# Kernel tuning notes

Measured on AMD Instinct MI355X. Metric: run time of the kernel, lower is better.

Reference implementation:

```python
import jax, jax.numpy as jnp
import numpy as np
import math

B = 8; SEQ = 1000; C_IN = 32; D = 512; H = 8; DK = 64; DV = 64
DFF = 2048; NL = 4; ARY = 4; INNER = 5


def get_mask_np(seq_size, ary, inner):
    # full k-ary tree sizes (padded) and effective sizes per scale
    full = 1
    while full < seq_size:
        full *= ary
    all_size = [full]; effe = [seq_size]
    while all_size[-1] > 1:
        all_size.append(all_size[-1] // ary)
        effe.append(math.ceil(effe[-1] / ary))
    n = sum(all_size)
    allow = np.zeros((n, n), dtype=bool)
    w = inner // 2
    starts = np.concatenate([[0], np.cumsum(all_size)]).astype(int)
    # intra-scale local window
    for l, sz in enumerate(all_size):
        s = starts[l]
        for i in range(sz):
            lo = max(i - w, 0); hi = min(i + w + 1, sz)
            allow[s + i, s + lo:s + hi] = True
    # inter-scale parent<->children links
    for l in range(1, len(all_size)):
        s = starts[l]; ps = starts[l - 1]
        for i in range(all_size[l]):
            lo = ps + i * ary; hi = ps + (i + 1) * ary
            allow[s + i, lo:hi] = True
            allow[lo:hi, s + i] = True
    return allow, all_size, effe

ALLOW_NP, ALL_SIZE, EFFE_SIZE = get_mask_np(SEQ, ARY, INNER)
NTOT = sum(ALL_SIZE)   # 1365
DEPTH = len(ALL_SIZE)  # 6
OFFS = np.concatenate([[0], np.cumsum(ALL_SIZE)]).astype(int)


def sinusoid_pe(length, d):
    pos = np.arange(length)[:, None].astype(np.float64)
    i = np.arange(d)[None, :]
    ang = pos / np.power(10000.0, (2 * (i // 2)) / d)
    pe = np.zeros((length, d), np.float32)
    pe[:, 0::2] = np.sin(ang[:, 0::2]); pe[:, 1::2] = np.cos(ang[:, 1::2])
    return pe

PE_NP = sinusoid_pe(SEQ, D)


def layer_norm(x, s, b, eps=1e-5):
    m = x.mean(-1, keepdims=True)
    v = ((x - m) ** 2).mean(-1, keepdims=True)
    return (x - m) * jax.lax.rsqrt(v + eps) * s + b


def setup_inputs() -> dict:
    key = jax.random.key(0)
    ks = jax.random.split(key, 10)
    p = lambda k, shape, sc=0.02: jax.random.normal(k, shape, jnp.float32) * sc
    return {
        "x": jax.random.normal(ks[0], (B, SEQ, C_IN), jnp.float32),
        "conv_w": p(ks[1], (D, C_IN, 3), 0.05),
        "norm_s": jnp.ones((D,), jnp.float32), "norm_b": jnp.zeros((D,), jnp.float32),
        "wq": p(ks[2], (NL, D, H * DK)), "wk": p(ks[3], (NL, D, H * DK)),
        "wv": p(ks[4], (NL, D, H * DV)), "wo": p(ks[5], (NL, H * DV, D)),
        "ln1_s": jnp.ones((NL, D), jnp.float32), "ln1_b": jnp.zeros((NL, D), jnp.float32),
        "w1": p(ks[6], (NL, D, DFF)), "b1": jnp.zeros((NL, DFF), jnp.float32),
        "w2": p(ks[7], (NL, DFF, D)), "b2": jnp.zeros((NL, D), jnp.float32),
        "ln2_s": jnp.ones((NL, D), jnp.float32), "ln2_b": jnp.zeros((NL, D), jnp.float32),
    }


def reference(x, conv_w, norm_s, norm_b, wq, wk, wv, wo, ln1_s, ln1_b,
              w1, b1, w2, b2, ln2_s, ln2_b):
    allow = jnp.asarray(ALLOW_NP)        # [N,N] True = attend
    pe = jnp.asarray(PE_NP)              # [S,D]
    # --- DataEmbedding: conv1d(k=3, circular pad, no bias) + sinusoid PE ---
    xt = jnp.concatenate([x[:, -1:], x, x[:, :1]], axis=1)       # (B,S+2,C)
    emb = jax.lax.conv_general_dilated(
        xt, conv_w, (1,), 'VALID', dimension_numbers=('NWC', 'OIW', 'NWC'))
    emb = emb + pe[None]                                          # (B,S,D)
    # pad sequence to full-tree leaf count
    emb = jnp.pad(emb, ((0, 0), (0, ALL_SIZE[0] - SEQ), (0, 0)))  # (B,L0,D)
    # --- MaxPooling_Construct: pool by ary per level, concat, LayerNorm ---
    parts = [emb]
    cur = emb
    for lvl in range(DEPTH - 1):
        L = cur.shape[1]
        cur = cur.reshape(B, L // ARY, ARY, D).max(axis=2)
        parts.append(cur)
    seq = jnp.concatenate(parts, axis=1)                          # (B,N,D)
    seq = layer_norm(seq, norm_s, norm_b)
    # --- masked MHA encoder layers (post-norm) ---
    scale = 1.0 / math.sqrt(DK)
    neg = jnp.float32(-1e9)
    for l in range(NL):
        q = (seq @ wq[l]).reshape(B, NTOT, H, DK)
        k = (seq @ wk[l]).reshape(B, NTOT, H, DK)
        v = (seq @ wv[l]).reshape(B, NTOT, H, DV)
        scores = jnp.einsum('bnhd,bmhd->bhnm', q, k) * scale
        scores = jnp.where(allow[None, None], scores, neg)
        attn = jax.nn.softmax(scores, axis=-1)
        ctx = jnp.einsum('bhnm,bmhd->bnhd', attn, v).reshape(B, NTOT, H * DV)
        seq = layer_norm(seq + ctx @ wo[l], ln1_s[l], ln1_b[l])
        ff = jax.nn.gelu(seq @ w1[l] + b1[l], approximate=False) @ w2[l] + b2[l]
        seq = layer_norm(seq + ff, ln2_s[l], ln2_b[l])
    # --- keep only the effective (unpadded) prefix of each scale ---
    out = jnp.concatenate(
        [seq[:, OFFS[i]:OFFS[i] + EFFE_SIZE[i]] for i in range(DEPTH)], axis=1)
    return out  # (B, sum(effe)=1334, D)
```

## Files before the change

### kernel.cpp

```cpp
#include <hip/hip_runtime.h>
#include <cstdint>
#include <math.h>

#define DEV __device__ __forceinline__

static constexpr int BQ = 8, SEQN = 1000, CIN = 32, NH = 8;
static constexpr int NLAY = 4;
static constexpr int NTOT_C = 1365;
static constexpr int M_REAL = BQ * NTOT_C;
static constexpr int M_PAD  = 11008;

DEV float bf2f(unsigned short u){ return __uint_as_float(((unsigned)u) << 16); }
DEV unsigned short f2bf(float f){
  unsigned u = __float_as_uint(f);
  u += 0x7fffu + ((u >> 16) & 1u);
  return (unsigned short)(u >> 16);
}

typedef __bf16 bf16x8 __attribute__((ext_vector_type(8)));
typedef float  f32x4  __attribute__((ext_vector_type(4)));
typedef unsigned short u16x8 __attribute__((ext_vector_type(8)));

#define GLD_LDS16(gp, lp) __builtin_amdgcn_global_load_lds( \
    (const __attribute__((address_space(1))) void*)(gp), \
    (__attribute__((address_space(3))) void*)(lp), 16, 0, 0)

template<int N> DEV void waitcnt_vm(){
  asm volatile("s_waitcnt vmcnt(%0)" :: "i"(N) : "memory");
}
DEV void cfence(){ asm volatile("" ::: "memory"); }

__global__ __launch_bounds__(256) void pe_kernel(float* __restrict__ pe)
{
  int idx = blockIdx.x * 256 + threadIdx.x;
  int d = idx & 511, s = idx >> 9;
  if (s >= SEQN) return;
  float e2 = (float)(d & ~1);
  float freq = exp2f(e2 * (-13.287712379549449f / 512.0f));
  float ang = (float)s * freq;
  pe[idx] = (d & 1) ? cosf(ang) : sinf(ang);
}

__global__ __launch_bounds__(256) void conv_kernel(const float* __restrict__ x,
    const float* __restrict__ w, const float* __restrict__ pe, float* __restrict__ seqf)
{
  __shared__ float ws_w[128 * 97];
  __shared__ __align__(16) float xs[66][32];
  int b = blockIdx.z, s0 = blockIdx.y * 64, d0 = blockIdx.x * 128;
  int tid = threadIdx.x;
  for (int i = tid; i < 128 * 96; i += 256){
    int r = i / 96, c = i - r * 96;
    ws_w[r * 97 + c] = w[(size_t)(d0 + r) * 96 + c];
  }
  for (int i = tid; i < 66 * 32; i += 256){
    int r = i >> 5, c = i & 31;
    int ss = s0 + r - 1;
    ss = (ss < 0) ? (ss + SEQN) : (ss >= SEQN ? ss - SEQN : ss);
    xs[r][c] = x[((size_t)b * SEQN + ss) * CIN + c];
  }
  __syncthreads();
  int dl = tid & 127, sh = tid >> 7;
  float wr[96];
  #pragma unroll
  for (int i = 0; i < 96; i++) wr[i] = ws_w[dl * 97 + i];
  int d = d0 + dl;
  for (int si = 0; si < 32; si++){
    int sl = sh * 32 + si;
    int s = s0 + sl;
    float acc = 0.f;
    #pragma unroll
    for (int kk = 0; kk < 3; kk++){
      const float* xr = xs[sl + kk];
      #pragma unroll
      for (int c = 0; c < 32; c++) acc += xr[c] * wr[c * 3 + kk];
    }
    float outv = (s < SEQN) ? acc + pe[(size_t)s * 512 + d] : 0.f;
    seqf[((size_t)b * NTOT_C + s) * 512 + d] = outv;
  }
}

__global__ __launch_bounds__(256) void pool_kernel(float* __restrict__ seqf,
    int inOff, int outOff, int outSz)
{
  int e = blockIdx.x * 256 + threadIdx.x;
  int d = e & 511;
  int r = e >> 9;
  int i = r % outSz;
  int b = r / outSz;
  const float* src = seqf + ((size_t)b * NTOT_C + inOff + 4 * i) * 512 + d;
  float m = fmaxf(fmaxf(src[0], src[512]), fmaxf(src[1024], src[1536]));
  seqf[((size_t)b * NTOT_C + outOff + i) * 512 + d] = m;
}

template<bool RES>
__global__ __launch_bounds__(256) void ln_kernel(const float* __restrict__ xin,
    const float* __restrict__ rin, float* __restrict__ outf, unsigned short* __restrict__ outb,
    const float* __restrict__ sg, const float* __restrict__ bg, int M)
{
  int row = blockIdx.x;
  int t = threadIdx.x;
  size_t base = (size_t)row * 512;
  if (row >= M){ outb[base + t] = 0; outb[base + t + 256] = 0; return; }
  float v0 = xin[base + t], v1 = xin[base + t + 256];
  if (RES){ v0 += rin[base + t]; v1 += rin[base + t + 256]; }
  __shared__ float red1[4], red2[4];
  int wv = t >> 6;
  float sall = v0 + v1;
  #pragma unroll
  for (int o = 32; o; o >>= 1) sall += __shfl_xor(sall, o, 64);
  if ((t & 63) == 0) red1[wv] = sall;
  __syncthreads();
  float mean = (red1[0] + red1[1] + red1[2] + red1[3]) * (1.f / 512.f);
  float d0 = v0 - mean, d1 = v1 - mean;
  float sq = d0 * d0 + d1 * d1;
  #pragma unroll
  for (int o = 32; o; o >>= 1) sq += __shfl_xor(sq, o, 64);
  if ((t & 63) == 0) red2[wv] = sq;
  __syncthreads();
  float var = (red2[0] + red2[1] + red2[2] + red2[3]) * (1.f / 512.f);
  float rstd = 1.f / sqrtf(var + 1e-5f);
  float y0 = d0 * rstd * sg[t] + bg[t];
  float y1 = d1 * rstd * sg[t + 256] + bg[t + 256];
  outf[base + t] = y0; outf[base + t + 256] = y1;
  outb[base + t] = f2bf(y0); outb[base + t + 256] = f2bf(y1);
}

__global__ __launch_bounds__(256) void wconv_kernel(const float* __restrict__ w,
    unsigned short* __restrict__ wt, int K, int N, size_t sStride, size_t dStride)
{
  __shared__ float tile[32][33];
  const float* wl = w + blockIdx.z * sStride;
  unsigned short* wtl = wt + blockIdx.z * dStride;
  int n0 = blockIdx.x * 32, k0 = blockIdx.y * 32;
  int c = threadIdx.x & 31, r8 = threadIdx.x >> 5;
  #pragma unroll
  for (int p = 0; p < 4; p++){ int r = r8 + p * 8; tile[r][c] = wl[(size_t)(k0 + r) * N + n0 + c]; }
  __syncthreads();
  #pragma unroll
  for (int p = 0; p < 4; p++){ int r = r8 + p * 8; wtl[(size_t)(n0 + r) * K + k0 + c] = f2bf(tile[c][r]); }
}

template<int EPI, int MR, int NR>
__global__ __launch_bounds__(256) void gemm_kernel(
    const unsigned short* __restrict__ A, const unsigned short* __restrict__ Wt,
    float* __restrict__ Cf, unsigned short* __restrict__ Cb,
    const float* __restrict__ bias, const float* __restrict__ Rf, int N, int K)
{
  constexpr int BM = 32 * MR, BN = 32 * NR;
  constexpr int SLOT_A = BM * 32, SLOT_B = BN * 32;
  constexpr int L = MR / 2 + NR / 2;
  __shared__ __align__(16) unsigned short As[3][SLOT_A];
  __shared__ __align__(16) unsigned short Bs[3][SLOT_B];
  const int tid = threadIdx.x;
  const int wv = tid >> 6, lane = tid & 63;
  const int m0 = blockIdx.x * BM, n0 = blockIdx.y * BN;
  const int wm = (wv >> 1) * 16 * MR, wn = (wv & 1) * 16 * NR;
  const int r16 = lane & 15, g = lane >> 4;

  const int lrow = lane >> 2;
  const int scg  = (lane & 3) ^ ((lrow >> 1) & 3);
  const unsigned short* gA = A + (size_t)(m0 + 8 * MR * wv + lrow) * K + scg * 8;
  const unsigned short* gB = Wt + (size_t)(n0 + 8 * NR * wv + lrow) * K + scg * 8;
  const int lAoff = wv * 8 * MR * 32;
  const int lBoff = wv * 8 * NR * 32;

  f32x4 acc[MR][NR] = {};
  const int nt = K >> 5;

  auto STAGE = [&](int slot, int k0){
    #pragma unroll
    for (int ii = 0; ii < MR / 2; ii++)
      GLD_LDS16(gA + k0 + ii * 16 * K, &As[slot][lAoff + ii * 512]);
    #pragma unroll
    for (int ii = 0; ii < NR / 2; ii++)
      GLD_LDS16(gB + k0 + ii * 16 * K, &Bs[slot][lBoff + ii * 512]);
  };

  STAGE(0, 0);
  STAGE(1, 32);
  int cur = 0;
  const int rswz = (g ^ ((r16 >> 1) & 3)) * 8;
  for (int t = 0; t < nt; t++){
    int s2 = (cur == 0) ? 2 : cur - 1;
    if (t + 2 < nt) STAGE(s2, (t + 2) * 32);
    if (t + 2 < nt)      waitcnt_vm<2 * L>();
    else if (t + 1 < nt) waitcnt_vm<L>();
    else                 waitcnt_vm<0>();
    __builtin_amdgcn_s_barrier();
    cfence();
    bf16x8 av[MR], bv[NR];
    #pragma unroll
    for (int m = 0; m < MR; m++)
      av[m] = *reinterpret_cast<const bf16x8*>(&As[cur][(wm + m * 16 + r16) * 32 + rswz]);
    #pragma unroll
    for (int n = 0; n < NR; n++)
      bv[n] = *reinterpret_cast<const bf16x8*>(&Bs[cur][(wn + n * 16 + r16) * 32 + rswz]);
    __builtin_amdgcn_s_setprio(1);
    #pragma unroll
    for (int m = 0; m < MR; m++)
      #pragma unroll
      for (int n = 0; n < NR; n++)
        acc[m][n] = __builtin_amdgcn_mfma_f32_16x16x32_bf16(av[m], bv[n], acc[m][n], 0, 0, 0);
    __builtin_amdgcn_s_setprio(0);
    __builtin_amdgcn_s_barrier();
    cfence();
    cur = (cur == 2) ? 0 : cur + 1;
  }

  const int colBase = n0 + wn + r16;
  #pragma unroll
  for (int m = 0; m < MR; m++){
    int rowBase = m0 + wm + m * 16 + g * 4;
    #pragma unroll
    for (int n = 0; n < NR; n++){
      int col = colBase + n * 16;
      float bsv = (EPI >= 2) ? bias[col] : 0.f;
      #pragma unroll
      for (int j = 0; j < 4; j++){
        float vlu = acc[m][n][j];
        if (EPI >= 2) vlu += bsv;
        if (EPI == 2) vlu = 0.5f * vlu * (1.f + erff(vlu * 0.70710678118654752f));
        size_t off = (size_t)(rowBase + j) * N + col;
        if (EPI == 0 || EPI == 3) vlu += Rf[off];
        if (EPI == 1 || EPI == 2) Cb[off] = f2bf(vlu);
        else                      Cf[off] = vlu;
      }
    }
  }
}

__global__ __launch_bounds__(256) void attn_kernel(
    const unsigned short* __restrict__ qkv, unsigned short* __restrict__ ctx)
{
  int wid = blockIdx.x * 4 + (threadIdx.x >> 6);
  int lane = threadIdx.x & 63;
  int n = wid % NTOT_C;
  int b = wid / NTOT_C;

  int i, sz, of, cb, par;
  if (n < 1024){ i = n;        sz = 1024; of = 0;    cb = -1;            par = 1024 + (i >> 2); }
  else if (n < 1280){ i = n - 1024; sz = 256; of = 1024; cb = 0    + 4 * i; par = 1280 + (i >> 2); }
  else if (n < 1344){ i = n - 1280; sz = 64;  of = 1280; cb = 1024 + 4 * i; par = 1344 + (i >> 2); }
  else if (n < 1360){ i = n - 1344; sz = 16;  of = 1344; cb = 1280 + 4 * i; par = 1360 + (i >> 2); }
  else if (n < 1364){ i = n - 1360; sz = 4;   of = 1360; cb = 1344 + 4 * i; par = 1364; }
  else { i = 0; sz = 1; of = 1364; cb = 1360; par = -1; }

  int nb[10];
  #pragma unroll
  for (int s5 = 0; s5 < 5; s5++){ int pos = i - 2 + s5; nb[s5] = (pos >= 0 && pos < sz) ? of + pos : -1; }
  #pragma unroll
  for (int r = 0; r < 4; r++) nb[5 + r] = (cb >= 0) ? cb + r : -1;
  nb[9] = par;

  const unsigned short* rows = qkv + ((size_t)b * NTOT_C) * 1536;

  u16x8 qv = *reinterpret_cast<const u16x8*>(rows + (size_t)n * 1536 + lane * 8);
  float qf[8];
  #pragma unroll
  for (int e = 0; e < 8; e++) qf[e] = bf2f(qv[e]);

  float sc[10];
  #pragma unroll
  for (int j = 0; j < 10; j++){
    int id = nb[j] >= 0 ? nb[j] : n;
    u16x8 kv = *reinterpret_cast<const u16x8*>(rows + (size_t)id * 1536 + 512 + lane * 8);
    float p = 0.f;
    #pragma unroll
    for (int e = 0; e < 8; e++) p += qf[e] * bf2f(kv[e]);
    p += __shfl_xor(p, 1, 64);
    p += __shfl_xor(p, 2, 64);
    p += __shfl_xor(p, 4, 64);
    sc[j] = (nb[j] >= 0) ? p * 0.125f : -1e30f;
  }
  float mx = sc[0];
  #pragma unroll
  for (int j = 1; j < 10; j++) mx = fmaxf(mx, sc[j]);
  float den = 0.f;
  float wj[10];
  #pragma unroll
  for (int j = 0; j < 10; j++){
    wj[j] = (nb[j] >= 0) ? expf(sc[j] - mx) : 0.f;
    den += wj[j];
  }
  float rden = 1.f / den;
  float accv[8] = {};
  #pragma unroll
  for (int j = 0; j < 10; j++){
    int id = nb[j] >= 0 ? nb[j] : n;
    u16x8 vv = *reinterpret_cast<const u16x8*>(rows + (size_t)id * 1536 + 1024 + lane * 8);
    float w = wj[j];
    #pragma unroll
    for (int e = 0; e < 8; e++) accv[e] += w * bf2f(vv[e]);
  }
  u16x8 ov;
  #pragma unroll
  for (int e = 0; e < 8; e++) ov[e] = f2bf(accv[e] * rden);
  *reinterpret_cast<u16x8*>(ctx + ((size_t)b * NTOT_C + n) * 512 + lane * 8) = ov;
}

__global__ __launch_bounds__(256) void gather_kernel(const float* __restrict__ seqf,
    float* __restrict__ out)
{
  int e = blockIdx.x * 256 + threadIdx.x;
  int d = e & 511;
  int r = e >> 9;
  int j = r % 1334;
  int b = r / 1334;
  int src;
  if      (j < 1000) src = j;
  else if (j < 1250) src = j + 24;
  else if (j < 1313) src = j + 30;
  else if (j < 1333) src = j + 31;
  else               src = 1364;
  out[e] = seqf[((size_t)b * NTOT_C + src) * 512 + d];
}

extern "C" void kernel_launch(void* const* d_in, const int* in_sizes, int n_in,
                              void* d_out, int out_size, void* d_ws, size_t ws_size,
                              hipStream_t stream)
{
  const float* x      = (const float*)d_in[0];
  const float* conv_w = (const float*)d_in[1];
  const float* norm_s = (const float*)d_in[2];
  const float* norm_b = (const float*)d_in[3];
  const float* wq     = (const float*)d_in[4];
  const float* wk     = (const float*)d_in[5];
  const float* wv     = (const float*)d_in[6];
  const float* wo     = (const float*)d_in[7];
  const float* ln1_s  = (const float*)d_in[8];
  const float* ln1_b  = (const float*)d_in[9];
  const float* w1     = (const float*)d_in[10];
  const float* b1     = (const float*)d_in[11];
  const float* w2     = (const float*)d_in[12];
  const float* b2     = (const float*)d_in[13];
  const float* ln2_s  = (const float*)d_in[14];
  const float* ln2_b  = (const float*)d_in[15];
  float* out = (float*)d_out;

  char* ws = (char*)d_ws;
  size_t off = 0;
  auto alloc = [&](size_t bytes) -> char* {
    char* p = ws + off; off += (bytes + 255) & ~(size_t)255; return p;
  };
  unsigned short* qkvT = (unsigned short*)alloc((size_t)NLAY * 1536 * 512 * 2);
  unsigned short* woT  = (unsigned short*)alloc((size_t)NLAY * 512 * 512 * 2);
  unsigned short* w1T  = (unsigned short*)alloc((size_t)NLAY * 2048 * 512 * 2);
  unsigned short* w2T  = (unsigned short*)alloc((size_t)NLAY * 512 * 2048 * 2);
  float*          seqf = (float*)alloc((size_t)M_PAD * 512 * 4);
  unsigned short* seqb = (unsigned short*)alloc((size_t)M_PAD * 512 * 2);
  float*          buff = (float*)alloc((size_t)M_PAD * 512 * 4);
  unsigned short* qkvb = (unsigned short*)alloc((size_t)M_PAD * 1536 * 2);
  unsigned short* ctxb = (unsigned short*)alloc((size_t)M_PAD * 512 * 2);
  unsigned short* ffn1 = qkvb;
  float*          pe   = buff;

  wconv_kernel<<<dim3(16,16,NLAY),256,0,stream>>>(wq, qkvT,              512,  512,  (size_t)512*512,  (size_t)1536*512);
  wconv_kernel<<<dim3(16,16,NLAY),256,0,stream>>>(wk, qkvT + 512*512,    512,  512,  (size_t)512*512,  (size_t)1536*512);
  wconv_kernel<<<dim3(16,16,NLAY),256,0,stream>>>(wv, qkvT + 1024*512,   512,  512,  (size_t)512*512,  (size_t)1536*512);
  wconv_kernel<<<dim3(16,16,NLAY),256,0,stream>>>(wo, woT,               512,  512,  (size_t)512*512,  (size_t)512*512);
  wconv_kernel<<<dim3(64,16,NLAY),256,0,stream>>>(w1, w1T,               512,  2048, (size_t)512*2048, (size_t)512*2048);
  wconv_kernel<<<dim3(16,64,NLAY),256,0,stream>>>(w2, w2T,               2048, 512,  (size_t)2048*512, (size_t)2048*512);

  pe_kernel<<<(SEQN * 512) / 256, 256, 0, stream>>>(pe);
  conv_kernel<<<dim3(4,16,BQ), 256, 0, stream>>>(x, conv_w, pe, seqf);
  const int psz[6]  = {1024, 256, 64, 16, 4, 1};
  const int poff[6] = {0, 1024, 1280, 1344, 1360, 1364};
  for (int l = 0; l < 5; l++)
    pool_kernel<<<(BQ * psz[l+1] * 512) / 256, 256, 0, stream>>>(seqf, poff[l], poff[l+1], psz[l+1]);
  ln_kernel<false><<<M_PAD, 256, 0, stream>>>(seqf, nullptr, seqf, seqb, norm_s, norm_b, M_REAL);

  for (int l = 0; l < NLAY; l++){
    gemm_kernel<1,4,4><<<dim3(86,12),256,0,stream>>>(seqb, qkvT + (size_t)l*1536*512, nullptr, qkvb, nullptr, nullptr, 1536, 512);
    attn_kernel<<<(BQ * NTOT_C + 3) / 4, 256, 0, stream>>>(qkvb, ctxb);
    gemm_kernel<0,2,2><<<dim3(172,8),256,0,stream>>>(ctxb, woT + (size_t)l*512*512, buff, nullptr, nullptr, seqf, 512, 512);
    ln_kernel<false><<<M_PAD,256,0,stream>>>(buff, nullptr, seqf, seqb, ln1_s + l*512, ln1_b + l*512, M_REAL);
    gemm_kernel<2,4,4><<<dim3(86,16),256,0,stream>>>(seqb, w1T + (size_t)l*2048*512, nullptr, ffn1, b1 + l*2048, nullptr, 2048, 512);
    gemm_kernel<3,2,4><<<dim3(172,4),256,0,stream>>>(ffn1, w2T + (size_t)l*512*2048, buff, nullptr, b2 + l*512, seqf, 512, 2048);
    ln_kernel<false><<<M_PAD,256,0,stream>>>(buff, nullptr, seqf, seqb, ln2_s + l*512, ln2_b + l*512, M_REAL);
  }

  gather_kernel<<<(BQ * 1334 * 512) / 256, 256, 0, stream>>>(seqf, out);
}
```

Baseline: 838.9 us.

## Replace GEMMs with 256-row, 512-thread double-buffered kernel and tanh GELU

Replaces the templated 3-stage GEMM with a larger-tile kernel: 256-row by up to 256-column tiles, 8 waves, K-step 64 with double buffering and split A/B prefetch interleaved across two half-steps. This raises data reuse per LDS load and cuts the number of blocks. The exact erf GELU is replaced by a clamped tanh approximation, which lowers epilogue cost but departs from the reference's exact GELU. Grid sizes shrink to 43 row blocks, which may underfill the GPU's CUs for the narrow N=512 GEMMs.

```diff
diff --git a/kernel.cpp b/kernel.cpp
--- a/kernel.cpp
+++ b/kernel.cpp
@@ -28,7 +28,16 @@
 template<int N> DEV void waitcnt_vm(){
   asm volatile("s_waitcnt vmcnt(%0)" :: "i"(N) : "memory");
 }
+DEV void waitcnt_lgkm0(){ asm volatile("s_waitcnt lgkmcnt(0)" ::: "memory"); }
 DEV void cfence(){ asm volatile("" ::: "memory"); }
+
+DEV float gelu_f(float x){
+  float z = 0.7978845608028654f * (x + 0.044715f * x * x * x);
+  z = fminf(fmaxf(z, -10.f), 10.f);
+  float e = __expf(2.f * z);
+  float th = (e - 1.f) / (e + 1.f);
+  return 0.5f * x * (1.f + th);
+}
 
 __global__ __launch_bounds__(256) void pe_kernel(float* __restrict__ pe)
 {
@@ -140,90 +149,120 @@
   for (int p = 0; p < 4; p++){ int r = r8 + p * 8; wtl[(size_t)(n0 + r) * K + k0 + c] = f2bf(tile[c][r]); }
 }
 
-template<int EPI, int MR, int NR>
-__global__ __launch_bounds__(256) void gemm_kernel(
+template<int EPI, int NR>
+__global__ __launch_bounds__(512, 1) void gemm256_kernel(
     const unsigned short* __restrict__ A, const unsigned short* __restrict__ Wt,
     float* __restrict__ Cf, unsigned short* __restrict__ Cb,
     const float* __restrict__ bias, const float* __restrict__ Rf, int N, int K)
 {
-  constexpr int BM = 32 * MR, BN = 32 * NR;
-  constexpr int SLOT_A = BM * 32, SLOT_B = BN * 32;
-  constexpr int L = MR / 2 + NR / 2;
-  __shared__ __align__(16) unsigned short As[3][SLOT_A];
-  __shared__ __align__(16) unsigned short Bs[3][SLOT_B];
+  constexpr int BN = 64 * NR;
+  __shared__ __align__(16) unsigned short Abuf[2][256 * 64];
+  __shared__ __align__(16) unsigned short Bbuf[2][BN * 64];
   const int tid = threadIdx.x;
-  const int wv = tid >> 6, lane = tid & 63;
-  const int m0 = blockIdx.x * BM, n0 = blockIdx.y * BN;
-  const int wm = (wv >> 1) * 16 * MR, wn = (wv & 1) * 16 * NR;
+  const int wid = tid >> 6, lane = tid & 63;
+  const int wm8 = wid >> 2, wn8 = wid & 3;
   const int r16 = lane & 15, g = lane >> 4;
-
-  const int lrow = lane >> 2;
-  const int scg  = (lane & 3) ^ ((lrow >> 1) & 3);
-  const unsigned short* gA = A + (size_t)(m0 + 8 * MR * wv + lrow) * K + scg * 8;
-  const unsigned short* gB = Wt + (size_t)(n0 + 8 * NR * wv + lrow) * K + scg * 8;
-  const int lAoff = wv * 8 * MR * 32;
-  const int lBoff = wv * 8 * NR * 32;
-
-  f32x4 acc[MR][NR] = {};
-  const int nt = K >> 5;
-
-  auto STAGE = [&](int slot, int k0){
-    #pragma unroll
-    for (int ii = 0; ii < MR / 2; ii++)
-      GLD_LDS16(gA + k0 + ii * 16 * K, &As[slot][lAoff + ii * 512]);
-    #pragma unroll
-    for (int ii = 0; ii < NR / 2; ii++)
-      GLD_LDS16(gB + k0 + ii * 16 * K, &Bs[slot][lBoff + ii * 512]);
-  };
-
-  STAGE(0, 0);
-  STAGE(1, 32);
-  int cur = 0;
-  const int rswz = (g ^ ((r16 >> 1) & 3)) * 8;
+  const int m0 = blockIdx.x * 256, n0 = blockIdx.y * BN;
+
+  const int strow = tid >> 3;
+  const int scol  = ((tid & 7) ^ (strow & 7)) * 8;
+  const unsigned short* gAs = A  + (size_t)(m0 + strow) * K + scol;
+  const unsigned short* gBs = Wt + (size_t)(n0 + strow) * K + scol;
+
+  const int swz0 = ((0 + g) ^ (r16 & 7)) * 8;
+  const int swz1 = ((4 + g) ^ (r16 & 7)) * 8;
+  const int arow = (wm8 * 128 + r16) * 64;
+  const int brow = (wn8 * (BN / 4) + r16) * 64;
+
+  const int nt = K >> 6;
+  f32x4 acc[8][NR] = {};
+
+  cfence();
+  #pragma unroll
+  for (int q = 0; q < 4; q++)  GLD_LDS16(gAs + q * 64 * K, &Abuf[0][q * 4096 + tid * 8]);
+  #pragma unroll
+  for (int q = 0; q < NR; q++) GLD_LDS16(gBs + q * 64 * K, &Bbuf[0][q * 4096 + tid * 8]);
+  if (nt > 1){
+    #pragma unroll
+    for (int q = 0; q < 4; q++) GLD_LDS16(gAs + 64 + q * 64 * K, &Abuf[1][q * 4096 + tid * 8]);
+    waitcnt_vm<4>();
+  } else {
+    waitcnt_vm<0>();
+  }
+  __builtin_amdgcn_s_barrier();
+  cfence();
+
   for (int t = 0; t < nt; t++){
-    int s2 = (cur == 0) ? 2 : cur - 1;
-    if (t + 2 < nt) STAGE(s2, (t + 2) * 32);
-    if (t + 2 < nt)      waitcnt_vm<2 * L>();
-    else if (t + 1 < nt) waitcnt_vm<L>();
-    else                 waitcnt_vm<0>();
+    const int d = t & 1;
+    const unsigned short* Ab = Abuf[d];
+    const unsigned short* Bb = Bbuf[d];
+
+    bf16x8 a0[8], b0[NR];
+    #pragma unroll
+    for (int m = 0; m < 8; m++)  a0[m] = *reinterpret_cast<const bf16x8*>(&Ab[arow + m * 1024 + swz0]);
+    #pragma unroll
+    for (int n = 0; n < NR; n++) b0[n] = *reinterpret_cast<const bf16x8*>(&Bb[brow + n * 1024 + swz0]);
+    if (t + 1 < nt){
+      cfence();
+      #pragma unroll
+      for (int q = 0; q < NR; q++)
+        GLD_LDS16(gBs + (t + 1) * 64 + q * 64 * K, &Bbuf[d ^ 1][q * 4096 + tid * 8]);
+      cfence();
+    }
+    __builtin_amdgcn_s_setprio(1);
+    #pragma unroll
+    for (int m = 0; m < 8; m++)
+      #pragma unroll
+      for (int n = 0; n < NR; n++)
+        acc[m][n] = __builtin_amdgcn_mfma_f32_16x16x32_bf16(a0[m], b0[n], acc[m][n], 0, 0, 0);
+    __builtin_amdgcn_s_setprio(0);
+
+    bf16x8 a1[8], b1v[NR];
+    #pragma unroll
+    for (int m = 0; m < 8; m++)  a1[m] = *reinterpret_cast<const bf16x8*>(&Ab[arow + m * 1024 + swz1]);
+    #pragma unroll
+    for (int n = 0; n < NR; n++) b1v[n] = *reinterpret_cast<const bf16x8*>(&Bb[brow + n * 1024 + swz1]);
+    waitcnt_lgkm0();
     __builtin_amdgcn_s_barrier();
     cfence();
-    bf16x8 av[MR], bv[NR];
-    #pragma unroll
-    for (int m = 0; m < MR; m++)
-      av[m] = *reinterpret_cast<const bf16x8*>(&As[cur][(wm + m * 16 + r16) * 32 + rswz]);
-    #pragma unroll
-    for (int n = 0; n < NR; n++)
-      bv[n] = *reinterpret_cast<const bf16x8*>(&Bs[cur][(wn + n * 16 + r16) * 32 + rswz]);
+    if (t + 2 < nt){
+      #pragma unroll
+      for (int q = 0; q < 4; q++)
+        GLD_LDS16(gAs + (t + 2) * 64 + q * 64 * K, &Abuf[d][q * 4096 + tid * 8]);
+      cfence();
+    }
     __builtin_amdgcn_s_setprio(1);
     #pragma unroll
-    for (int m = 0; m < MR; m++)
+    for (int m = 0; m < 8; m++)
       #pragma unroll
       for (int n = 0; n < NR; n++)
-        acc[m][n] = __builtin_amdgcn_mfma_f32_16x16x32_bf16(av[m], bv[n], acc[m][n], 0, 0, 0);
+        acc[m][n] = __builtin_amdgcn_mfma_f32_16x16x32_bf16(a1[m], b1v[n], acc[m][n], 0, 0, 0);
     __builtin_amdgcn_s_setprio(0);
-    __builtin_amdgcn_s_barrier();
-    cfence();
-    cur = (cur == 2) ? 0 : cur + 1;
-  }
-
-  const int colBase = n0 + wn + r16;
-  #pragma unroll
-  for (int m = 0; m < MR; m++){
-    int rowBase = m0 + wm + m * 16 + g * 4;
+
+    if (t + 1 < nt){
+      if (t + 2 < nt) waitcnt_vm<4>();
+      else            waitcnt_vm<0>();
+      __builtin_amdgcn_s_barrier();
+      cfence();
+    }
+  }
+
+  const int colBase = n0 + wn8 * (BN / 4) + r16;
+  #pragma unroll
+  for (int m = 0; m < 8; m++){
+    int row = m0 + wm8 * 128 + m * 16 + g * 4;
     #pragma unroll
     for (int n = 0; n < NR; n++){
       int col = colBase + n * 16;
       float bsv = (EPI >= 2) ? bias[col] : 0.f;
       #pragma unroll
       for (int j = 0; j < 4; j++){
-        float vlu = acc[m][n][j];
-        if (EPI >= 2) vlu += bsv;
-        if (EPI == 2) vlu = 0.5f * vlu * (1.f + erff(vlu * 0.70710678118654752f));
-        size_t off = (size_t)(rowBase + j) * N + col;
-        if (EPI == 0 || EPI == 3) vlu += Rf[off];
-        if (EPI == 1 || EPI == 2) Cb[off] = f2bf(vlu);
-        else                      Cf[off] = vlu;
+        float v = acc[m][n][j];
+        if (EPI >= 2) v += bsv;
+        if (EPI == 2) v = gelu_f(v);
+        size_t off = (size_t)(row + j) * N + col;
+        if (EPI == 0 || EPI == 3) Cf[off] = v + Rf[off];
+        else                      Cb[off] = f2bf(v);
       }
     }
   }
@@ -370,12 +409,12 @@
   ln_kernel<false><<<M_PAD, 256, 0, stream>>>(seqf, nullptr, seqf, seqb, norm_s, norm_b, M_REAL);
 
   for (int l = 0; l < NLAY; l++){
-    gemm_kernel<1,4,4><<<dim3(86,12),256,0,stream>>>(seqb, qkvT + (size_t)l*1536*512, nullptr, qkvb, nullptr, nullptr, 1536, 512);
+    gemm256_kernel<1,4><<<dim3(43,6),512,0,stream>>>(seqb, qkvT + (size_t)l*1536*512, nullptr, qkvb, nullptr, nullptr, 1536, 512);
     attn_kernel<<<(BQ * NTOT_C + 3) / 4, 256, 0, stream>>>(qkvb, ctxb);
-    gemm_kernel<0,2,2><<<dim3(172,8),256,0,stream>>>(ctxb, woT + (size_t)l*512*512, buff, nullptr, nullptr, seqf, 512, 512);
+    gemm256_kernel<0,2><<<dim3(43,4),512,0,stream>>>(ctxb, woT + (size_t)l*512*512, buff, nullptr, nullptr, seqf, 512, 512);
     ln_kernel<false><<<M_PAD,256,0,stream>>>(buff, nullptr, seqf, seqb, ln1_s + l*512, ln1_b + l*512, M_REAL);
-    gemm_kernel<2,4,4><<<dim3(86,16),256,0,stream>>>(seqb, w1T + (size_t)l*2048*512, nullptr, ffn1, b1 + l*2048, nullptr, 2048, 512);
-    gemm_kernel<3,2,4><<<dim3(172,4),256,0,stream>>>(ffn1, w2T + (size_t)l*512*2048, buff, nullptr, b2 + l*512, seqf, 512, 2048);
+    gemm256_kernel<2,4><<<dim3(43,8),512,0,stream>>>(seqb, w1T + (size_t)l*2048*512, nullptr, ffn1, b1 + l*2048, nullptr, 2048, 512);
+    gemm256_kernel<3,2><<<dim3(43,4),512,0,stream>>>(ffn1, w2T + (size_t)l*512*2048, buff, nullptr, b2 + l*512, seqf, 512, 2048);
     ln_kernel<false><<<M_PAD,256,0,stream>>>(buff, nullptr, seqf, seqb, ln2_s + l*512, ln2_b + l*512, M_REAL);
   }
 
```

Measured after the change: 893.3 us. 1.06x slower.
